# Kernel tuning notes

Hardware: AMD Instinct MI355X
Metric: run time of the kernel (lower is better)

The kernel has to match this reference:

```python
import jax, jax.numpy as jnp
import numpy as np

# (multiplicity, irrep_dim) for irreps_in == irreps_out: 128x0e + 64x1o + 32x2e
IRREPS = [(128, 1), (64, 3), (32, 5)]
NUM_INDICES = 64
N_ELEMENTS = 8192
SCALE = 1.0  # module's `scale` arg; total coeff = scale / sqrt(num_indices) / sqrt(mul_in)
W_DIM = sum(m * m for m, _ in IRREPS)  # 21504


def setup_inputs() -> dict:
    key = jax.random.key(0)
    ks = jax.random.split(key, 5)
    x0 = jax.random.normal(ks[0], (N_ELEMENTS, 128, 1), jnp.float32)
    x1 = jax.random.normal(ks[1], (N_ELEMENTS, 64, 3), jnp.float32)
    x2 = jax.random.normal(ks[2], (N_ELEMENTS, 32, 5), jnp.float32)
    w = jax.random.normal(ks[3], (NUM_INDICES, W_DIM), jnp.float32)
    # Random contiguous segment sizes that sum exactly to N_ELEMENTS:
    bnd = jnp.sort(jax.random.randint(ks[4], (NUM_INDICES - 1,), 0, N_ELEMENTS + 1)).astype(jnp.int32)
    counts = jnp.diff(jnp.concatenate([jnp.zeros((1,), jnp.int32), bnd,
                                       jnp.full((1,), N_ELEMENTS, jnp.int32)]))
    return {"x0": x0, "x1": x1, "x2": x2, "w": w, "num_index_counts": counts}


def reference(x0, x1, x2, w, num_index_counts):
    """Indexed (segmented) equivariant linear: rows are grouped contiguously by
    num_index_counts; segment g uses weight row w[g]. Per matched irrep the
    weight block is a (mul_in, mul_out) mixing matrix applied identically to
    each of the ir.dim components (Schur's lemma), with fan-in normalization
    1/sqrt(mul_in) (cue.descriptors.linear) times scale/sqrt(num_indices)."""
    n = x0.shape[0]
    # segment id per row (rows are already grouped contiguously, as in Repeats())
    sid = jnp.repeat(jnp.arange(NUM_INDICES), num_index_counts, total_repeat_length=n)
    xs = (x0, x1, x2)
    ys = []
    off = 0
    for xk, (mul, ir_dim) in zip(xs, IRREPS):
        blk = w[:, off:off + mul * mul].reshape(NUM_INDICES, mul, mul)  # (E, m_in, m_out)
        coeff = float(SCALE / np.sqrt(NUM_INDICES) / np.sqrt(mul))
        wk = blk[sid]  # (n, m_in, m_out) per-row weight gather
        # y[n, o, i] = coeff * sum_m x[n, m, i] * w[g(n), m, o]
        ys.append(coeff * jnp.einsum('nmi,nmo->noi', xk, wk))
        off += mul * mul
    return tuple(ys)
```

## Files before the change

### kernel.cpp

```cpp
#include <hip/hip_runtime.h>

#define NSEG 64
#define NROW 8192
#define TILE 16
#define WROW 21504
#define NBLK 576

#define PT0 20
#define P1  196
#define P2  164

__global__ __launch_bounds__(256) void iil_kernel(
    const float* __restrict__ x0, const float* __restrict__ x1, const float* __restrict__ x2,
    const float* __restrict__ w, const int* __restrict__ counts,
    float* __restrict__ y0, float* __restrict__ y1, float* __restrict__ y2)
{
    __shared__ float xT0[128 * PT0];
    __shared__ float sx1[TILE * P1];
    __shared__ float sx2[TILE * P2];
    __shared__ float w1s[64 * 64];
    __shared__ int sstart[NSEG + 1];
    __shared__ int tstart[NSEG + 1];

    const int t = threadIdx.x;

    if (t < NSEG) {
        int c = counts[t];
        int v = c;
        #pragma unroll
        for (int d = 1; d < NSEG; d <<= 1) {
            int u = __shfl_up(v, d, 64);
            if (t >= d) v += u;
        }
        sstart[t + 1] = v;
        int tcv = (c + TILE - 1) >> 4;
        #pragma unroll
        for (int d = 1; d < NSEG; d <<= 1) {
            int u = __shfl_up(tcv, d, 64);
            if (t >= d) tcv += u;
        }
        tstart[t + 1] = tcv;
        if (t == 0) { sstart[0] = 0; tstart[0] = 0; }
    }
    __syncthreads();

    const int b = blockIdx.x;
    if (b >= tstart[NSEG]) return;

    int lo = 0, hi = NSEG;
    while (hi - lo > 1) {
        int mid = (lo + hi) >> 1;
        if (tstart[mid] <= b) lo = mid; else hi = mid;
    }
    const int g = lo;
    const int s = sstart[g] + (b - tstart[g]) * TILE;
    const int nr = min(TILE, sstart[g + 1] - s);
    const float* __restrict__ wseg = w + (size_t)g * WROW;

    {
        const float4 z4 = make_float4(0.f, 0.f, 0.f, 0.f);
        const float4* g0 = (const float4*)x0 + (size_t)s * 32;
        #pragma unroll
        for (int i = 0; i < 2; ++i) {
            int idx = t + i * 256;
            int r = idx >> 5, c4 = idx & 31;
            float4 v = (r < nr) ? g0[idx] : z4;
            xT0[(c4 * 4 + 0) * PT0 + r] = v.x;
            xT0[(c4 * 4 + 1) * PT0 + r] = v.y;
            xT0[(c4 * 4 + 2) * PT0 + r] = v.z;
            xT0[(c4 * 4 + 3) * PT0 + r] = v.w;
        }
        const float4* g1 = (const float4*)x1 + (size_t)s * 48;
        #pragma unroll
        for (int i = 0; i < 3; ++i) {
            int idx = t + i * 256;
            int r = idx / 48, c = idx - r * 48;
            float4 v = (r < nr) ? g1[idx] : z4;
            *(float4*)(sx1 + r * P1 + c * 4) = v;
        }
        const float4* g2 = (const float4*)x2 + (size_t)s * 40;
        #pragma unroll
        for (int i = 0; i < 3; ++i) {
            int idx = t + i * 256;
            if (idx < 640) {
                int r = idx / 40, c = idx - r * 40;
                float4 v = (r < nr) ? g2[idx] : z4;
                *(float4*)(sx2 + r * P2 + c * 4) = v;
            }
        }
        const float4* gw1 = (const float4*)(wseg + 16384);
        #pragma unroll
        for (int i = 0; i < 4; ++i) {
            int idx = t + i * 256;
            *(float4*)(w1s + idx * 4) = gw1[idx];
        }
    }
    __syncthreads();

    {
        const int og = t & 63;
        const int rg = t >> 6;
        const float* wp = wseg + og * 2;
        const float* xb = xT0 + rg * 4;
        float acc[8];
        #pragma unroll
        for (int i = 0; i < 8; ++i) acc[i] = 0.f;
        #pragma unroll 4
        for (int k = 0; k < 128; ++k) {
            float4 xv = *(const float4*)(xb + k * PT0);
            float2 wv = *(const float2*)(wp + (size_t)k * 128);
            acc[0] = fmaf(xv.x, wv.x, acc[0]);
            acc[1] = fmaf(xv.x, wv.y, acc[1]);
            acc[2] = fmaf(xv.y, wv.x, acc[2]);
            acc[3] = fmaf(xv.y, wv.y, acc[3]);
            acc[4] = fmaf(xv.z, wv.x, acc[4]);
            acc[5] = fmaf(xv.z, wv.y, acc[5]);
            acc[6] = fmaf(xv.w, wv.x, acc[6]);
            acc[7] = fmaf(xv.w, wv.y, acc[7]);
        }
        const float c0 = 0.011048543456039806f;
        #pragma unroll
        for (int jr = 0; jr < 4; ++jr) {
            int r = rg * 4 + jr;
            if (r < nr) {
                float2 v = make_float2(acc[jr * 2] * c0, acc[jr * 2 + 1] * c0);
                *(float2*)(y0 + (size_t)(s + r) * 128 + og * 2) = v;
            }
        }
    }

    {
        const int og = t & 15;
        const int r = t >> 4;
        const float* xrow = sx1 + r * P1;
        float acc[12];
        #pragma unroll
        for (int i = 0; i < 12; ++i) acc[i] = 0.f;
        #pragma unroll 2
        for (int kq = 0; kq < 16; ++kq) {
            float4 xq0 = *(const float4*)(xrow + 12 * kq + 0);
            float4 xq1 = *(const float4*)(xrow + 12 * kq + 4);
            float4 xq2 = *(const float4*)(xrow + 12 * kq + 8);
            float xf[12] = {xq0.x, xq0.y, xq0.z, xq0.w,
                            xq1.x, xq1.y, xq1.z, xq1.w,
                            xq2.x, xq2.y, xq2.z, xq2.w};
            #pragma unroll
            for (int kk = 0; kk < 4; ++kk) {
                int k = 4 * kq + kk;
                float4 wv = *(const float4*)(w1s + k * 64 + og * 4);
                #pragma unroll
                for (int oo = 0; oo < 4; ++oo) {
                    float wvo = (oo == 0) ? wv.x : (oo == 1) ? wv.y : (oo == 2) ? wv.z : wv.w;
                    acc[oo * 3 + 0] = fmaf(wvo, xf[kk * 3 + 0], acc[oo * 3 + 0]);
                    acc[oo * 3 + 1] = fmaf(wvo, xf[kk * 3 + 1], acc[oo * 3 + 1]);
                    acc[oo * 3 + 2] = fmaf(wvo, xf[kk * 3 + 2], acc[oo * 3 + 2]);
                }
            }
        }
        const float c1 = 0.015625f;
        if (r < nr) {
            float* yb = y1 + (size_t)(s + r) * 192 + og * 12;
            *(float4*)(yb + 0) = make_float4(acc[0] * c1, acc[1] * c1, acc[2] * c1, acc[3] * c1);
            *(float4*)(yb + 4) = make_float4(acc[4] * c1, acc[5] * c1, acc[6] * c1, acc[7] * c1);
            *(float4*)(yb + 8) = make_float4(acc[8] * c1, acc[9] * c1, acc[10] * c1, acc[11] * c1);
        }
    }

    {
        const int og = t & 15;
        const int r = t >> 4;
        const float* xrow = sx2 + r * P2;
        const float* wp = wseg + 20480 + og * 2;
        float acc[10];
        #pragma unroll
        for (int i = 0; i < 10; ++i) acc[i] = 0.f;
        #pragma unroll
        for (int kq = 0; kq < 8; ++kq) {
            float xf[20];
            #pragma unroll
            for (int j = 0; j < 5; ++j) {
                float4 v = *(const float4*)(xrow + 20 * kq + 4 * j);
                xf[4 * j + 0] = v.x; xf[4 * j + 1] = v.y; xf[4 * j + 2] = v.z; xf[4 * j + 3] = v.w;
            }
            #pragma unroll
            for (int kk = 0; kk < 4; ++kk) {
                int k = 4 * kq + kk;
                float2 wv = *(const float2*)(wp + (size_t)k * 32);
                #pragma unroll
                for (int i = 0; i < 5; ++i) {
                    acc[i]     = fmaf(wv.x, xf[5 * kk + i], acc[i]);
                    acc[5 + i] = fmaf(wv.y, xf[5 * kk + i], acc[5 + i]);
                }
            }
        }
        const float c2 = 0.022097086912079608f;
        if (r < nr) {
            float* yb = y2 + (size_t)(s + r) * 160 + og * 10;
            #pragma unroll
            for (int i = 0; i < 5; ++i) {
                *(float2*)(yb + 2 * i) = make_float2(acc[2 * i] * c2, acc[2 * i + 1] * c2);
            }
        }
    }
}

extern "C" void kernel_launch(void* const* d_in, const int* in_sizes, int n_in,
                              void* d_out, int out_size, void* d_ws, size_t ws_size,
                              hipStream_t stream) {
    const float* x0 = (const float*)d_in[0];
    const float* x1 = (const float*)d_in[1];
    const float* x2 = (const float*)d_in[2];
    const float* w  = (const float*)d_in[3];
    const int* counts = (const int*)d_in[4];

    float* y0 = (float*)d_out;
    float* y1 = y0 + (size_t)NROW * 128;
    float* y2 = y1 + (size_t)NROW * 192;

    hipLaunchKernelGGL(iil_kernel, dim3(NBLK), dim3(256), 0, stream,
                       x0, x1, x2, w, counts, y0, y1, y2);
}
```

Measured before the change: 111.6 us.

## Split each tile's three irrep GEMMs into separate blocks with shared LDS buffer

The grid triples, so each block handles only one irrep (0e, 1o or 2e) for its 16-row tile instead of all three in sequence. The three blocks share a single small LDS buffer, which cuts shared memory per block and should raise occupancy and parallelism. The 1o weight block is now read straight from global or cache rather than staged in LDS, and the 0e thread mapping changes to 4 outputs by 2 rows. The cost is the segment prefix scan and search repeated in three times as many blocks, plus more global weight traffic per block.

After: 96.59 us. 13.4% less time.

```diff
diff --git a/kernel.cpp b/kernel.cpp
--- a/kernel.cpp
+++ b/kernel.cpp
@@ -4,8 +4,7 @@
 #define NROW 8192
 #define TILE 16
 #define WROW 21504
-#define NBLK 576
-
+#define NBPP 576
 #define PT0 20
 #define P1  196
 #define P2  164
@@ -15,10 +14,7 @@
     const float* __restrict__ w, const int* __restrict__ counts,
     float* __restrict__ y0, float* __restrict__ y1, float* __restrict__ y2)
 {
-    __shared__ float xT0[128 * PT0];
-    __shared__ float sx1[TILE * P1];
-    __shared__ float sx2[TILE * P2];
-    __shared__ float w1s[64 * 64];
+    __shared__ float sbuf[TILE * P1];
     __shared__ int sstart[NSEG + 1];
     __shared__ int tstart[NSEG + 1];
 
@@ -33,32 +29,34 @@
             if (t >= d) v += u;
         }
         sstart[t + 1] = v;
-        int tcv = (c + TILE - 1) >> 4;
+        int tc = (c + TILE - 1) >> 4;
         #pragma unroll
         for (int d = 1; d < NSEG; d <<= 1) {
-            int u = __shfl_up(tcv, d, 64);
-            if (t >= d) tcv += u;
-        }
-        tstart[t + 1] = tcv;
+            int u = __shfl_up(tc, d, 64);
+            if (t >= d) tc += u;
+        }
+        tstart[t + 1] = tc;
         if (t == 0) { sstart[0] = 0; tstart[0] = 0; }
     }
     __syncthreads();
 
-    const int b = blockIdx.x;
-    if (b >= tstart[NSEG]) return;
+    const int phase = blockIdx.x / NBPP;
+    const int pb = blockIdx.x - phase * NBPP;
+    if (pb >= tstart[NSEG]) return;
 
     int lo = 0, hi = NSEG;
     while (hi - lo > 1) {
         int mid = (lo + hi) >> 1;
-        if (tstart[mid] <= b) lo = mid; else hi = mid;
+        if (tstart[mid] <= pb) lo = mid; else hi = mid;
     }
     const int g = lo;
-    const int s = sstart[g] + (b - tstart[g]) * TILE;
+    const int s = sstart[g] + (pb - tstart[g]) * TILE;
     const int nr = min(TILE, sstart[g + 1] - s);
     const float* __restrict__ wseg = w + (size_t)g * WROW;
-
-    {
-        const float4 z4 = make_float4(0.f, 0.f, 0.f, 0.f);
+    const float4 z4 = make_float4(0.f, 0.f, 0.f, 0.f);
+
+    if (phase == 0) {
+        float* xT0 = sbuf;
         const float4* g0 = (const float4*)x0 + (size_t)s * 32;
         #pragma unroll
         for (int i = 0; i < 2; ++i) {
@@ -70,6 +68,37 @@
             xT0[(c4 * 4 + 2) * PT0 + r] = v.z;
             xT0[(c4 * 4 + 3) * PT0 + r] = v.w;
         }
+        __syncthreads();
+        const int og = t & 31;
+        const int rg = t >> 5;
+        const float* wp = wseg + og * 4;
+        const float* xb = xT0 + rg * 2;
+        float acc[8];
+        #pragma unroll
+        for (int i = 0; i < 8; ++i) acc[i] = 0.f;
+        #pragma unroll 8
+        for (int k = 0; k < 128; ++k) {
+            float2 xv = *(const float2*)(xb + k * PT0);
+            float4 wv = *(const float4*)(wp + (size_t)k * 128);
+            acc[0] = fmaf(xv.x, wv.x, acc[0]);
+            acc[1] = fmaf(xv.x, wv.y, acc[1]);
+            acc[2] = fmaf(xv.x, wv.z, acc[2]);
+            acc[3] = fmaf(xv.x, wv.w, acc[3]);
+            acc[4] = fmaf(xv.y, wv.x, acc[4]);
+            acc[5] = fmaf(xv.y, wv.y, acc[5]);
+            acc[6] = fmaf(xv.y, wv.z, acc[6]);
+            acc[7] = fmaf(xv.y, wv.w, acc[7]);
+        }
+        const float c0 = 0.011048543456039806f;
+        int r0 = rg * 2;
+        if (r0 < nr)
+            *(float4*)(y0 + (size_t)(s + r0) * 128 + og * 4) =
+                make_float4(acc[0] * c0, acc[1] * c0, acc[2] * c0, acc[3] * c0);
+        if (r0 + 1 < nr)
+            *(float4*)(y0 + (size_t)(s + r0 + 1) * 128 + og * 4) =
+                make_float4(acc[4] * c0, acc[5] * c0, acc[6] * c0, acc[7] * c0);
+    } else if (phase == 1) {
+        float* sx1 = sbuf;
         const float4* g1 = (const float4*)x1 + (size_t)s * 48;
         #pragma unroll
         for (int i = 0; i < 3; ++i) {
@@ -78,61 +107,11 @@
             float4 v = (r < nr) ? g1[idx] : z4;
             *(float4*)(sx1 + r * P1 + c * 4) = v;
         }
-        const float4* g2 = (const float4*)x2 + (size_t)s * 40;
-        #pragma unroll
-        for (int i = 0; i < 3; ++i) {
-            int idx = t + i * 256;
-            if (idx < 640) {
-                int r = idx / 40, c = idx - r * 40;
-                float4 v = (r < nr) ? g2[idx] : z4;
-                *(float4*)(sx2 + r * P2 + c * 4) = v;
-            }
-        }
-        const float4* gw1 = (const float4*)(wseg + 16384);
-        #pragma unroll
-        for (int i = 0; i < 4; ++i) {
-            int idx = t + i * 256;
-            *(float4*)(w1s + idx * 4) = gw1[idx];
-        }
-    }
-    __syncthreads();
-
-    {
-        const int og = t & 63;
-        const int rg = t >> 6;
-        const float* wp = wseg + og * 2;
-        const float* xb = xT0 + rg * 4;
-        float acc[8];
-        #pragma unroll
-        for (int i = 0; i < 8; ++i) acc[i] = 0.f;
-        #pragma unroll 4
-        for (int k = 0; k < 128; ++k) {
-            float4 xv = *(const float4*)(xb + k * PT0);
-            float2 wv = *(const float2*)(wp + (size_t)k * 128);
-            acc[0] = fmaf(xv.x, wv.x, acc[0]);
-            acc[1] = fmaf(xv.x, wv.y, acc[1]);
-            acc[2] = fmaf(xv.y, wv.x, acc[2]);
-            acc[3] = fmaf(xv.y, wv.y, acc[3]);
-            acc[4] = fmaf(xv.z, wv.x, acc[4]);
-            acc[5] = fmaf(xv.z, wv.y, acc[5]);
-            acc[6] = fmaf(xv.w, wv.x, acc[6]);
-            acc[7] = fmaf(xv.w, wv.y, acc[7]);
-        }
-        const float c0 = 0.011048543456039806f;
-        #pragma unroll
-        for (int jr = 0; jr < 4; ++jr) {
-            int r = rg * 4 + jr;
-            if (r < nr) {
-                float2 v = make_float2(acc[jr * 2] * c0, acc[jr * 2 + 1] * c0);
-                *(float2*)(y0 + (size_t)(s + r) * 128 + og * 2) = v;
-            }
-        }
-    }
-
-    {
+        __syncthreads();
         const int og = t & 15;
         const int r = t >> 4;
         const float* xrow = sx1 + r * P1;
+        const float* wp = wseg + 16384 + og * 4;
         float acc[12];
         #pragma unroll
         for (int i = 0; i < 12; ++i) acc[i] = 0.f;
@@ -146,8 +125,7 @@
                             xq2.x, xq2.y, xq2.z, xq2.w};
             #pragma unroll
             for (int kk = 0; kk < 4; ++kk) {
-                int k = 4 * kq + kk;
-                float4 wv = *(const float4*)(w1s + k * 64 + og * 4);
+                float4 wv = *(const float4*)(wp + (size_t)(4 * kq + kk) * 64);
                 #pragma unroll
                 for (int oo = 0; oo < 4; ++oo) {
                     float wvo = (oo == 0) ? wv.x : (oo == 1) ? wv.y : (oo == 2) ? wv.z : wv.w;
@@ -164,9 +142,19 @@
             *(float4*)(yb + 4) = make_float4(acc[4] * c1, acc[5] * c1, acc[6] * c1, acc[7] * c1);
             *(float4*)(yb + 8) = make_float4(acc[8] * c1, acc[9] * c1, acc[10] * c1, acc[11] * c1);
         }
-    }
-
-    {
+    } else {
+        float* sx2 = sbuf;
+        const float4* g2 = (const float4*)x2 + (size_t)s * 40;
+        #pragma unroll
+        for (int i = 0; i < 3; ++i) {
+            int idx = t + i * 256;
+            if (idx < 640) {
+                int r = idx / 40, c = idx - r * 40;
+                float4 v = (r < nr) ? g2[idx] : z4;
+                *(float4*)(sx2 + r * P2 + c * 4) = v;
+            }
+        }
+        __syncthreads();
         const int og = t & 15;
         const int r = t >> 4;
         const float* xrow = sx2 + r * P2;
@@ -184,8 +172,7 @@
             }
             #pragma unroll
             for (int kk = 0; kk < 4; ++kk) {
-                int k = 4 * kq + kk;
-                float2 wv = *(const float2*)(wp + (size_t)k * 32);
+                float2 wv = *(const float2*)(wp + (size_t)(4 * kq + kk) * 32);
                 #pragma unroll
                 for (int i = 0; i < 5; ++i) {
                     acc[i]     = fmaf(wv.x, xf[5 * kk + i], acc[i]);
@@ -197,9 +184,8 @@
         if (r < nr) {
             float* yb = y2 + (size_t)(s + r) * 160 + og * 10;
             #pragma unroll
-            for (int i = 0; i < 5; ++i) {
+            for (int i = 0; i < 5; ++i)
                 *(float2*)(yb + 2 * i) = make_float2(acc[2 * i] * c2, acc[2 * i + 1] * c2);
-            }
         }
     }
 }
@@ -217,6 +203,6 @@
     float* y1 = y0 + (size_t)NROW * 128;
     float* y2 = y1 + (size_t)NROW * 192;
 
-    hipLaunchKernelGGL(iil_kernel, dim3(NBLK), dim3(256), 0, stream,
+    hipLaunchKernelGGL(iil_kernel, dim3(3 * NBPP), dim3(256), 0, stream,
                        x0, x1, x2, w, counts, y0, y1, y2);
 }
```
